# Kernel optimization log

Measured on AMD Instinct MI355X. Metric: run time of the kernel, lower is better.

## Reference

```python
import jax, jax.numpy as jnp
import numpy as np

B, T, IN_CH = 64, 128, 32
H, C = 1, 4
STRIDE = (H, C)
OUT_CH = 4
CHANNELS = (IN_CH - C) // STRIDE[1] + 1  # 8
SIG_DEPTH = 4
D = CHANNELS + 1  # +1 time channel -> 9
LAYERS = (512, 256)
OUT_DIM = 10
SIG_CHANNELS = sum(D ** k for k in range(1, SIG_DEPTH + 1))  # 7380


def _signature(path, depth):
    """Truncated path signature (basepoint=True). path: [N, L, d] -> [N, sum_k d^k].
    Chen's identity scan: S <- S (tensor-mult) exp(dx), levels kept flattened."""
    N, L, d = path.shape
    # basepoint=True: path is prepended with zeros, so first increment is path[:, 0]
    inc = jnp.concatenate([path[:, :1], jnp.diff(path, axis=1)], axis=1)  # [N, L, d]
    inc = jnp.transpose(inc, (1, 0, 2))  # [L, N, d] scan axis first

    def chen_step(S, dx):
        # exponential of the increment: E_k = dx^{\otimes k} / k!
        E = [dx]
        for k in range(2, depth + 1):
            E.append((E[-1][:, :, None] * dx[:, None, :]).reshape(N, -1) / k)
        # Chen: S'_k = S_k + E_k + sum_{j=1}^{k-1} S_j (x) E_{k-j}
        newS = []
        for k in range(1, depth + 1):
            acc = S[k - 1] + E[k - 1]
            for j in range(1, k):
                acc = acc + (S[j - 1][:, :, None] * E[k - 1 - j][:, None, :]).reshape(N, -1)
            newS.append(acc)
        return tuple(newS), None

    S0 = tuple(jnp.zeros((N, d ** k), path.dtype) for k in range(1, depth + 1))
    S, _ = jax.lax.scan(chen_step, S0, inc)
    return jnp.concatenate(S, axis=1)  # [N, SIG_CHANNELS]


def _forward(x, conv_w, conv_b, w0, b0, w1, b1, w2, b2):
    y = jax.lax.conv_general_dilated(
        x, conv_w, window_strides=STRIDE, padding='VALID',
        dimension_numbers=('NCHW', 'OIHW', 'NCHW'))
    y = y + conv_b[None, :, None, None]            # [B, OUT_CH, T', CHANNELS]
    Tp = y.shape[2]
    y = y.reshape(-1, Tp, CHANNELS)                # [B*OUT_CH, T', CHANNELS]
    # signatory.Augment(layer_sizes=(), include_time=True): prepend time channel
    time = jnp.broadcast_to(
        jnp.linspace(0.0, 1.0, Tp, dtype=y.dtype)[None, :, None],
        (y.shape[0], Tp, 1))
    y = jnp.concatenate([time, y], axis=2)         # [B*OUT_CH, T', D]
    sig = _signature(y, SIG_DEPTH)                 # [B*OUT_CH, SIG_CHANNELS]
    z = sig.reshape(-1, OUT_CH * SIG_CHANNELS)     # [B, OUT_CH*SIG_CHANNELS]
    z = jax.nn.sigmoid(z @ w0 + b0)                # dropout = identity (eval mode)
    z = jax.nn.sigmoid(z @ w1 + b1)
    return jax.nn.log_softmax(z @ w2 + b2, axis=1)


def setup_inputs() -> dict:
    key = jax.random.key(0)
    ks = jax.random.split(key, 8)
    x = jax.random.normal(ks[0], (B, 1, T, IN_CH), jnp.float32)
    conv_w = jax.random.normal(ks[1], (OUT_CH, 1, H, C), jnp.float32) * (2.0 / (H * C)) ** 0.5
    conv_b = jnp.zeros((OUT_CH,), jnp.float32)
    dims = [OUT_CH * SIG_CHANNELS] + list(LAYERS) + [OUT_DIM]
    out = {"x": x, "conv_w": conv_w, "conv_b": conv_b}
    for i in range(3):
        out[f"w{i}"] = jax.random.normal(ks[2 + i], (dims[i], dims[i + 1]), jnp.float32) * (2.0 / dims[i]) ** 0.5
        out[f"b{i}"] = jnp.zeros((dims[i + 1],), jnp.float32)
    return out


def reference(x, conv_w, conv_b, w0, b0, w1, b1, w2, b2):
    return _forward(x, conv_w, conv_b, w0, b0, w1, b1, w2, b2)
```

## Files before the change

### kernel.cpp

```cpp
#include <hip/hip_runtime.h>
#include <hip/hip_bf16.h>
#include <math.h>

#define TT 128
#define IN_CH 32
#define NPATH 256
#define SIGCH 7380
#define K1 29520
#define N1 512
#define N2 256

typedef __attribute__((ext_vector_type(8))) short bf16x8;
typedef __attribute__((ext_vector_type(4))) float f32x4;

static __device__ __forceinline__ unsigned pack2bf(float a, float b) {
    union { __hip_bfloat162 h2; unsigned u; } cv;
    cv.h2.x = __float2bfloat16(a);
    cv.h2.y = __float2bfloat16(b);
    return cv.u;
}

__global__ __launch_bounds__(512, 1) void sig_kernel(const float* __restrict__ x,
        const float* __restrict__ cw, const float* __restrict__ cb,
        float* __restrict__ sig ) {
    __shared__ float incT[9][132];
    __shared__ __align__(16) float sb1[12];
    __shared__ __align__(16) float sb2[9][12];
    __shared__ __align__(16) float sb3[81][12];
    __shared__ __align__(16) float sb4[729][12];
    const int p = blockIdx.x;
    const int b = p >> 2, oc = p & 3;
    const int tid = threadIdx.x;

    const float4 wv = *(const float4*)(cw + oc * 4);
    const float bias = cb[oc];
    const float* xb = x + (long)b * TT * IN_CH;

    for (int it = tid; it < TT * 8; it += 512) {
        const int t = it >> 3, ch = it & 7;
        const float4 xa = *(const float4*)(xb + t * IN_CH + ch * 4);
        float v = xa.x * wv.x + xa.y * wv.y + xa.z * wv.z + xa.w * wv.w + bias;
        if (t > 0) {
            const float4 xm = *(const float4*)(xb + (t - 1) * IN_CH + ch * 4);
            v -= xm.x * wv.x + xm.y * wv.y + xm.z * wv.z + xm.w * wv.w + bias;
        }
        incT[1 + ch][t] = v;
    }
    if (tid < TT) incT[0][tid] = tid ? (1.f / 127.f) : 0.f;
    __syncthreads();

    const int g = tid >> 8;
    const int gtid = tid & 255;
    const bool act = gtid < 243;
    const int base3 = 3 * gtid;
    const int i1 = base3 / 81;
    const int i2 = (base3 / 9) % 9;
    const int i30 = base3 % 9;

    float S4[3][9] = {};
    float s3[3] = {0.f, 0.f, 0.f};
    float s2 = 0.f, s1 = 0.f;

#define LD(R, T4) (*(const float4*)&incT[(R)][(T4)])
#define STEP4(CMP) do { \
    const float E1 = e1v.CMP, E2 = e2v.CMP; \
    const float F0 = f0v.CMP, F1 = f1v.CMP, F2 = f2v.CMP; \
    const float t12 = E1 * E2; \
    const float s1d2 = s1 * E2; \
    const float Ak = t12 * (1.f / 24.f) + s1d2 * (1.f / 6.f) + s2 * 0.5f; \
    const float Bk = t12 * (1.f / 6.f) + s1d2 * 0.5f + s2; \
    const float K0 = F0 * Ak + s3[0]; \
    const float K1v = F1 * Ak + s3[1]; \
    const float K2v = F2 * Ak + s3[2]; \
    _Pragma("unroll") \
    for (int c = 0; c < 9; ++c) { \
        const float Ac = A4[c].CMP; \
        S4[0][c] += K0 * Ac; S4[1][c] += K1v * Ac; S4[2][c] += K2v * Ac; \
    } \
    s3[0] += Bk * F0; s3[1] += Bk * F1; s3[2] += Bk * F2; \
    s2 += E2 * (0.5f * E1 + s1); \
    s1 += E1; \
} while (0)

    if (act) {
        const int t0g = g * 64;
        for (int gg = 0; gg < 16; ++gg) {
            const int t4 = t0g + gg * 4;
            float4 A4[9];
#pragma unroll
            for (int c = 0; c < 9; ++c) A4[c] = LD(c, t4);
            const float4 e1v = LD(i1, t4), e2v = LD(i2, t4);
            const float4 f0v = LD(i30, t4), f1v = LD(i30 + 1, t4), f2v = LD(i30 + 2, t4);
            STEP4(x); STEP4(y); STEP4(z); STEP4(w);
        }
    }
#undef STEP4
#undef LD

    if (act && g == 1) {
        if (i2 == 0 && i30 == 0) sb1[i1] = s1;
        if (i30 == 0) sb2[i1][i2] = s2;
#pragma unroll
        for (int q = 0; q < 3; ++q) sb3[i1 * 9 + i2][i30 + q] = s3[q];
#pragma unroll
        for (int q = 0; q < 3; ++q)
#pragma unroll
            for (int c = 0; c < 9; ++c) sb4[base3 + q][c] = S4[q][c];
    }
    __syncthreads();

    if (act && g == 0) {
        float S1B[9];
#pragma unroll
        for (int c = 0; c < 9; ++c) S1B[c] = sb1[c];
#pragma unroll
        for (int q = 0; q < 3; ++q) {
            const float* r2 = sb2[i30 + q];
            const float* r3 = sb3[i2 * 9 + i30 + q];
            const float* r4 = sb4[base3 + q];
#pragma unroll
            for (int c = 0; c < 9; ++c)
                S4[q][c] += s3[q] * S1B[c] + s2 * r2[c] + s1 * r3[c] + r4[c];
        }
#pragma unroll
        for (int q = 0; q < 3; ++q)
            s3[q] += s2 * S1B[i30 + q] + s1 * sb2[i2][i30 + q] + sb3[i1 * 9 + i2][i30 + q];
        s2 += s1 * S1B[i2] + sb2[i1][i2];
        s1 += S1B[i1];

        float* sp = sig + (long)p * SIGCH;
        if (i2 == 0 && i30 == 0) sp[i1] = s1;
        if (i30 == 0) sp[9 + base3 / 9] = s2;
        sp[90 + base3 + 0] = s3[0];
        sp[90 + base3 + 1] = s3[1];
        sp[90 + base3 + 2] = s3[2];
#pragma unroll
        for (int q = 0; q < 3; q++)
#pragma unroll
            for (int l = 0; l < 9; l++)
                sp[819 + (base3 + q) * 9 + l] = S4[q][l];
    }
}

__global__ __launch_bounds__(256) void gemm1_kernel(const float* __restrict__ zsig,
        const float* __restrict__ w0, float* __restrict__ part, int nsub) {
    __shared__ unsigned short za[64][136];
    __shared__ unsigned short wb[64][136];
    const int nq = blockIdx.x;
    const int kc = blockIdx.y;
    const int n0 = nq * 64;
    const int tid = threadIdx.x;
    const int lane = tid & 63;
    const int wvid = __builtin_amdgcn_readfirstlane(tid >> 6);
    const int r0 = wvid * 16;
    const int rA = lane & 15, gr = lane >> 4;

    {
        const int row = tid >> 2, off = 120 + 2 * (tid & 3);
        *(unsigned*)&za[row][off] = 0u;
        *(unsigned*)&wb[row][off] = 0u;
    }

    f32x4 acc[4];
#pragma unroll
    for (int t = 0; t < 4; ++t) acc[t] = (f32x4){0.f, 0.f, 0.f, 0.f};

    for (int s = 0; s < nsub; ++s) {
        const int kb = (blockIdx.y * nsub + s) * 120;
        if (s) __syncthreads();
#pragma unroll
        for (int j = 0; j < 16; ++j) {
            const int i = tid + j * 256;
            const int row = i >> 6, kp = i & 63;
            if (kp < 60) {
                const float2 v = *(const float2*)(zsig + (long)row * K1 + kb + 2 * kp);
                *(unsigned*)&za[row][2 * kp] = pack2bf(v.x, v.y);
            }
        }
#pragma unroll
        for (int j = 0; j < 16; ++j) {
            const int i = tid + j * 256;
            const int c = i & 63, kq = i >> 6;
            if (kq < 60) {
                const float a = w0[(long)(kb + 2 * kq) * N1 + n0 + c];
                const float bvl = w0[(long)(kb + 2 * kq + 1) * N1 + n0 + c];
                *(unsigned*)&wb[c][2 * kq] = pack2bf(a, bvl);
            }
        }
        __syncthreads();
#pragma unroll
        for (int ks = 0; ks < 4; ++ks) {
            const bf16x8 af = *(const bf16x8*)&za[r0 + rA][ks * 32 + gr * 8];
#pragma unroll
            for (int t = 0; t < 4; ++t) {
                const bf16x8 bf = *(const bf16x8*)&wb[16 * t + rA][ks * 32 + gr * 8];
                acc[t] = __builtin_amdgcn_mfma_f32_16x16x32_bf16(af, bf, acc[t], 0, 0, 0);
            }
        }
    }

    float* pp = part + ((long)blockIdx.y * 64 + r0 + 4 * gr) * N1 + n0 + rA;
#pragma unroll
    for (int t = 0; t < 4; ++t)
#pragma unroll
        for (int j = 0; j < 4; ++j)
            pp[(long)j * N1 + 16 * t] = acc[t][j];
}

__global__ __launch_bounds__(256) void red1_kernel(const float* __restrict__ part,
        const float* __restrict__ b0v, float* __restrict__ z1, int ksplit) {
    __shared__ float4 red[256];
    const int tid = threadIdx.x;
    const int cellL = tid & 15, slice = tid >> 4;
    const int cell = blockIdx.x * 16 + cellL;
    const int per = (ksplit + 15) >> 4;
    const int ks = slice * per, ke = min(ksplit, ks + per);
    float4 a = make_float4(0.f, 0.f, 0.f, 0.f);
    for (int kc = ks; kc < ke; kc++) {
        const float4 pv = *(const float4*)(part + ((long)kc * 8192 + cell) * 4);
        a.x += pv.x; a.y += pv.y; a.z += pv.z; a.w += pv.w;
    }
    red[tid] = a;
    __syncthreads();
    if (tid < 128) { float4 o = red[tid + 128]; red[tid].x += o.x; red[tid].y += o.y; red[tid].z += o.z; red[tid].w += o.w; }
    __syncthreads();
    if (tid < 64) { float4 o = red[tid + 64]; red[tid].x += o.x; red[tid].y += o.y; red[tid].z += o.z; red[tid].w += o.w; }
    __syncthreads();
    if (tid < 32) { float4 o = red[tid + 32]; red[tid].x += o.x; red[tid].y += o.y; red[tid].z += o.z; red[tid].w += o.w; }
    __syncthreads();
    if (tid < 16) {
        float4 sum = red[tid];
        float4 o = red[tid + 16];
        sum.x += o.x; sum.y += o.y; sum.z += o.z; sum.w += o.w;
        const float4 bv = *(const float4*)(b0v + (cell & 127) * 4);
        float4 r;
        r.x = 1.f / (1.f + expf(-(sum.x + bv.x)));
        r.y = 1.f / (1.f + expf(-(sum.y + bv.y)));
        r.z = 1.f / (1.f + expf(-(sum.z + bv.z)));
        r.w = 1.f / (1.f + expf(-(sum.w + bv.w)));
        *(float4*)(z1 + cell * 4) = r;
    }
}

__global__ __launch_bounds__(256) void gemm2_kernel(const float* __restrict__ z1,
        const float* __restrict__ w1, const float* __restrict__ b1v,
        float* __restrict__ z2) {
    __shared__ float red[256];
    const int m = blockIdx.x >> 2, nq = blockIdx.x & 3;
    const int tid = threadIdx.x;
    const int c = tid & 63, s = tid >> 6;
    const int n = nq * 64 + c;
    const float* zr = z1 + m * N1 + s * 128;
    const float* wr = w1 + (long)(s * 128) * N2 + n;
    float acc = 0.f;
#pragma unroll 16
    for (int k = 0; k < 128; k++) acc += zr[k] * wr[(long)k * N2];
    red[tid] = acc;
    __syncthreads();
    if (tid < 128) red[tid] += red[tid + 128];
    __syncthreads();
    if (tid < 64) {
        float sum = red[tid] + red[tid + 64] + b1v[n];
        z2[m * N2 + n] = 1.f / (1.f + expf(-sum));
    }
}

__global__ __launch_bounds__(64) void head_kernel(const float* __restrict__ z2,
        const float* __restrict__ w2, const float* __restrict__ b2v,
        float* __restrict__ out) {
    const int m = blockIdx.x;
    const int tid = threadIdx.x;
    __shared__ float logits[10];
    if (tid < 10) {
        float s = b2v[tid];
        const float* zr = z2 + m * N2;
#pragma unroll 8
        for (int k = 0; k < N2; k++) s += zr[k] * w2[k * 10 + tid];
        logits[tid] = s;
    }
    __syncthreads();
    if (tid == 0) {
        float mx = logits[0];
        for (int j = 1; j < 10; j++) mx = fmaxf(mx, logits[j]);
        float sum = 0.f;
        for (int j = 0; j < 10; j++) sum += expf(logits[j] - mx);
        const float lse = mx + logf(sum);
        for (int j = 0; j < 10; j++) out[m * 10 + j] = logits[j] - lse;
    }
}

extern "C" void kernel_launch(void* const* d_in, const int* in_sizes, int n_in,
                              void* d_out, int out_size, void* d_ws, size_t ws_size,
                              hipStream_t stream) {
    const float* x  = (const float*)d_in[0];
    const float* cw = (const float*)d_in[1];
    const float* cb = (const float*)d_in[2];
    const float* w0 = (const float*)d_in[3];
    const float* b0 = (const float*)d_in[4];
    const float* w1 = (const float*)d_in[5];
    const float* b1 = (const float*)d_in[6];
    const float* w2 = (const float*)d_in[7];
    const float* b2 = (const float*)d_in[8];

    const size_t fixed = (size_t)NPATH * SIGCH + 64 * N1 + 64 * N2;
    int ksplit = 41, nsub = 6;
    if (ws_size >= (fixed + (size_t)123 * 64 * N1) * 4)      { ksplit = 123; nsub = 2; }
    else if (ws_size >= (fixed + (size_t)82 * 64 * N1) * 4)  { ksplit = 82;  nsub = 3; }

    float* ws   = (float*)d_ws;
    float* sigb = ws;
    float* part = sigb + (long)NPATH * SIGCH;
    float* z1   = part + (long)ksplit * 64 * N1;
    float* z2   = z1 + 64 * N1;
    float* out  = (float*)d_out;

    sig_kernel<<<NPATH, 512, 0, stream>>>(x, cw, cb, sigb);
    gemm1_kernel<<<dim3(8, ksplit), 256, 0, stream>>>(sigb, w0, part, nsub);
    red1_kernel<<<512, 256, 0, stream>>>(part, b0, z1, ksplit);
    gemm2_kernel<<<256, 256, 0, stream>>>(z1, w1, b1, z2);
    head_kernel<<<64, 64, 0, stream>>>(z2, w2, b2, out);
}
```

Measured before the change: 68.83 us.

## Split signature scan into four time chunks merged via Chen identity kernel

The single per-path signature kernel, which split time into two halves across 512 threads, is replaced by a scan kernel over four 32-step time chunks (1024 blocks of 256 threads) that writes partial signatures to workspace. A new merge kernel then combines the four partials sequentially with Chen's identity. This aims to raise parallelism and occupancy across the GPU's compute units, at the cost of an extra launch, extra global traffic for partial signatures, and three merge rounds instead of one. Workspace use grows, which may push the gemm split choice toward a smaller ksplit.

```diff
diff --git a/kernel.cpp b/kernel.cpp
--- a/kernel.cpp
+++ b/kernel.cpp
@@ -6,6 +6,7 @@
 #define IN_CH 32
 #define NPATH 256
 #define SIGCH 7380
+#define SIGP 7392
 #define K1 29520
 #define N1 512
 #define N2 256
@@ -20,37 +21,35 @@
     return cv.u;
 }
 
-__global__ __launch_bounds__(512, 1) void sig_kernel(const float* __restrict__ x,
+__global__ __launch_bounds__(256) void sigscan_kernel(const float* __restrict__ x,
         const float* __restrict__ cw, const float* __restrict__ cb,
-        float* __restrict__ sig ) {
-    __shared__ float incT[9][132];
-    __shared__ __align__(16) float sb1[12];
-    __shared__ __align__(16) float sb2[9][12];
-    __shared__ __align__(16) float sb3[81][12];
-    __shared__ __align__(16) float sb4[729][12];
+        float* __restrict__ psig ) {
+    __shared__ float incT[9][36];
     const int p = blockIdx.x;
+    const int q4 = blockIdx.y;
     const int b = p >> 2, oc = p & 3;
     const int tid = threadIdx.x;
 
     const float4 wv = *(const float4*)(cw + oc * 4);
     const float bias = cb[oc];
     const float* xb = x + (long)b * TT * IN_CH;
-
-    for (int it = tid; it < TT * 8; it += 512) {
-        const int t = it >> 3, ch = it & 7;
+    const int t0 = q4 * 32;
+
+    {
+        const int tl = tid >> 3, ch = tid & 7;
+        const int t = t0 + tl;
         const float4 xa = *(const float4*)(xb + t * IN_CH + ch * 4);
         float v = xa.x * wv.x + xa.y * wv.y + xa.z * wv.z + xa.w * wv.w + bias;
         if (t > 0) {
             const float4 xm = *(const float4*)(xb + (t - 1) * IN_CH + ch * 4);
             v -= xm.x * wv.x + xm.y * wv.y + xm.z * wv.z + xm.w * wv.w + bias;
         }
-        incT[1 + ch][t] = v;
-    }
-    if (tid < TT) incT[0][tid] = tid ? (1.f / 127.f) : 0.f;
-    __syncthreads();
-
-    const int g = tid >> 8;
-    const int gtid = tid & 255;
+        incT[1 + ch][tl] = v;
+        if (tid < 32) incT[0][tid] = (t0 + tid) ? (1.f / 127.f) : 0.f;
+    }
+    __syncthreads();
+
+    const int gtid = tid;
     const bool act = gtid < 243;
     const int base3 = 3 * gtid;
     const int i1 = base3 / 81;
@@ -83,9 +82,8 @@
 } while (0)
 
     if (act) {
-        const int t0g = g * 64;
-        for (int gg = 0; gg < 16; ++gg) {
-            const int t4 = t0g + gg * 4;
+        for (int gg = 0; gg < 8; ++gg) {
+            const int t4 = gg * 4;
             float4 A4[9];
 #pragma unroll
             for (int c = 0; c < 9; ++c) A4[c] = LD(c, t4);
@@ -93,41 +91,78 @@
             const float4 f0v = LD(i30, t4), f1v = LD(i30 + 1, t4), f2v = LD(i30 + 2, t4);
             STEP4(x); STEP4(y); STEP4(z); STEP4(w);
         }
+        float* d = psig + (long)(p * 4 + q4) * SIGP;
+        if (i2 == 0 && i30 == 0) d[i1] = s1;
+        if (i30 == 0) d[9 + i1 * 9 + i2] = s2;
+        d[90 + base3 + 0] = s3[0];
+        d[90 + base3 + 1] = s3[1];
+        d[90 + base3 + 2] = s3[2];
+#pragma unroll
+        for (int qq = 0; qq < 3; ++qq)
+#pragma unroll
+            for (int c = 0; c < 9; ++c)
+                d[819 + (base3 + qq) * 9 + c] = S4[qq][c];
     }
 #undef STEP4
 #undef LD
-
-    if (act && g == 1) {
-        if (i2 == 0 && i30 == 0) sb1[i1] = s1;
-        if (i30 == 0) sb2[i1][i2] = s2;
-#pragma unroll
-        for (int q = 0; q < 3; ++q) sb3[i1 * 9 + i2][i30 + q] = s3[q];
-#pragma unroll
-        for (int q = 0; q < 3; ++q)
-#pragma unroll
-            for (int c = 0; c < 9; ++c) sb4[base3 + q][c] = S4[q][c];
-    }
-    __syncthreads();
-
-    if (act && g == 0) {
-        float S1B[9];
-#pragma unroll
-        for (int c = 0; c < 9; ++c) S1B[c] = sb1[c];
-#pragma unroll
-        for (int q = 0; q < 3; ++q) {
-            const float* r2 = sb2[i30 + q];
-            const float* r3 = sb3[i2 * 9 + i30 + q];
-            const float* r4 = sb4[base3 + q];
+}
+
+__global__ __launch_bounds__(256) void sigmerge_kernel(const float* __restrict__ psig,
+        float* __restrict__ sig ) {
+    __shared__ float sbuf[SIGP];
+    const int p = blockIdx.x;
+    const int tid = threadIdx.x;
+    const bool act = tid < 243;
+    const int base3 = 3 * tid;
+    const int i1 = base3 / 81;
+    const int i2 = (base3 / 9) % 9;
+    const int i30 = base3 % 9;
+
+    float S4[3][9];
+    float s3[3], s2 = 0.f, s1 = 0.f;
+
+    const float* pA = psig + (long)(p * 4) * SIGP;
+    if (act) {
+        s1 = pA[i1];
+        s2 = pA[9 + i1 * 9 + i2];
+#pragma unroll
+        for (int qq = 0; qq < 3; ++qq) s3[qq] = pA[90 + base3 + qq];
+#pragma unroll
+        for (int qq = 0; qq < 3; ++qq)
 #pragma unroll
             for (int c = 0; c < 9; ++c)
-                S4[q][c] += s3[q] * S1B[c] + s2 * r2[c] + s1 * r3[c] + r4[c];
-        }
-#pragma unroll
-        for (int q = 0; q < 3; ++q)
-            s3[q] += s2 * S1B[i30 + q] + s1 * sb2[i2][i30 + q] + sb3[i1 * 9 + i2][i30 + q];
-        s2 += s1 * S1B[i2] + sb2[i1][i2];
-        s1 += S1B[i1];
-
+                S4[qq][c] = pA[819 + (base3 + qq) * 9 + c];
+    }
+
+    for (int r = 1; r < 4; ++r) {
+        __syncthreads();
+        const float* pB = psig + (long)(p * 4 + r) * SIGP;
+        for (int i = tid; i < SIGP / 4; i += 256)
+            *(float4*)&sbuf[i * 4] = *(const float4*)(pB + i * 4);
+        __syncthreads();
+        if (act) {
+            float S1B[9];
+#pragma unroll
+            for (int c = 0; c < 9; ++c) S1B[c] = sbuf[c];
+#pragma unroll
+            for (int qq = 0; qq < 3; ++qq) {
+                const float* r2 = &sbuf[9 + (i30 + qq) * 9];
+                const float* r3 = &sbuf[90 + (i2 * 9 + i30 + qq) * 9];
+                const float* r4 = &sbuf[819 + (base3 + qq) * 9];
+#pragma unroll
+                for (int c = 0; c < 9; ++c)
+                    S4[qq][c] += s3[qq] * S1B[c] + s2 * r2[c] + s1 * r3[c] + r4[c];
+            }
+#pragma unroll
+            for (int qq = 0; qq < 3; ++qq)
+                s3[qq] += s2 * S1B[i30 + qq] + s1 * sbuf[9 + i2 * 9 + i30 + qq]
+                        + sbuf[90 + (i1 * 9 + i2) * 9 + i30 + qq];
+            s2 += s1 * S1B[i2] + sbuf[9 + i1 * 9 + i2];
+            s1 += S1B[i1];
+        }
+    }
+
+    if (act) {
         float* sp = sig + (long)p * SIGCH;
         if (i2 == 0 && i30 == 0) sp[i1] = s1;
         if (i30 == 0) sp[9 + base3 / 9] = s2;
@@ -135,10 +170,10 @@
         sp[90 + base3 + 1] = s3[1];
         sp[90 + base3 + 2] = s3[2];
 #pragma unroll
-        for (int q = 0; q < 3; q++)
+        for (int qq = 0; qq < 3; qq++)
 #pragma unroll
             for (int l = 0; l < 9; l++)
-                sp[819 + (base3 + q) * 9 + l] = S4[q][l];
+                sp[819 + (base3 + qq) * 9 + l] = S4[qq][l];
     }
 }
 
@@ -147,7 +182,6 @@
     __shared__ unsigned short za[64][136];
     __shared__ unsigned short wb[64][136];
     const int nq = blockIdx.x;
-    const int kc = blockIdx.y;
     const int n0 = nq * 64;
     const int tid = threadIdx.x;
     const int lane = tid & 63;
@@ -302,19 +336,22 @@
     const float* w2 = (const float*)d_in[7];
     const float* b2 = (const float*)d_in[8];
 
-    const size_t fixed = (size_t)NPATH * SIGCH + 64 * N1 + 64 * N2;
+    const size_t fixed = (size_t)NPATH * SIGCH + (size_t)NPATH * 4 * SIGP
+                       + 64 * N1 + 64 * N2;
     int ksplit = 41, nsub = 6;
     if (ws_size >= (fixed + (size_t)123 * 64 * N1) * 4)      { ksplit = 123; nsub = 2; }
     else if (ws_size >= (fixed + (size_t)82 * 64 * N1) * 4)  { ksplit = 82;  nsub = 3; }
 
     float* ws   = (float*)d_ws;
     float* sigb = ws;
-    float* part = sigb + (long)NPATH * SIGCH;
+    float* psig = sigb + (long)NPATH * SIGCH;
+    float* part = psig + (long)NPATH * 4 * SIGP;
     float* z1   = part + (long)ksplit * 64 * N1;
     float* z2   = z1 + 64 * N1;
     float* out  = (float*)d_out;
 
-    sig_kernel<<<NPATH, 512, 0, stream>>>(x, cw, cb, sigb);
+    sigscan_kernel<<<dim3(NPATH, 4), 256, 0, stream>>>(x, cw, cb, psig);
+    sigmerge_kernel<<<NPATH, 256, 0, stream>>>(psig, sigb);
     gemm1_kernel<<<dim3(8, ksplit), 256, 0, stream>>>(sigb, w0, part, nsub);
     red1_kernel<<<512, 256, 0, stream>>>(part, b0, z1, ksplit);
     gemm2_kernel<<<256, 256, 0, stream>>>(z1, w1, b1, z2);
```

Measured after the change: 83.56 us. 21.4% more time.

## Store signatures as bf16, vectorize gemm1 loads, fuse gemm2 and head

Applied to the files above, without the earlier changes.

The signature kernel now writes its output as bf16 instead of fp32. This halves the intermediate buffer and lets gemm1 copy 16-byte chunks straight into shared memory without a per-element convert. The w0 staging now uses float4 loads across columns instead of scalar loads. gemm2 and the head are merged into one tail kernel per batch row, which saves a launch and the z2 round trip but gives each block a longer serial loop over k. The bf16 rounding now happens earlier, which matches the rounding gemm1 already applied.

```diff
diff --git a/kernel.cpp b/kernel.cpp
--- a/kernel.cpp
+++ b/kernel.cpp
@@ -11,6 +11,7 @@
 #define N2 256
 
 typedef __attribute__((ext_vector_type(8))) short bf16x8;
+typedef __attribute__((ext_vector_type(8))) unsigned short u16x8;
 typedef __attribute__((ext_vector_type(4))) float f32x4;
 
 static __device__ __forceinline__ unsigned pack2bf(float a, float b) {
@@ -22,7 +23,7 @@
 
 __global__ __launch_bounds__(512, 1) void sig_kernel(const float* __restrict__ x,
         const float* __restrict__ cw, const float* __restrict__ cb,
-        float* __restrict__ sig ) {
+        __hip_bfloat16* __restrict__ sigbf ) {
     __shared__ float incT[9][132];
     __shared__ __align__(16) float sb1[12];
     __shared__ __align__(16) float sb2[9][12];
@@ -128,26 +129,25 @@
         s2 += s1 * S1B[i2] + sb2[i1][i2];
         s1 += S1B[i1];
 
-        float* sp = sig + (long)p * SIGCH;
-        if (i2 == 0 && i30 == 0) sp[i1] = s1;
-        if (i30 == 0) sp[9 + base3 / 9] = s2;
-        sp[90 + base3 + 0] = s3[0];
-        sp[90 + base3 + 1] = s3[1];
-        sp[90 + base3 + 2] = s3[2];
+        __hip_bfloat16* sp = sigbf + (long)p * SIGCH;
+        if (i2 == 0 && i30 == 0) sp[i1] = __float2bfloat16(s1);
+        if (i30 == 0) sp[9 + base3 / 9] = __float2bfloat16(s2);
+        sp[90 + base3 + 0] = __float2bfloat16(s3[0]);
+        sp[90 + base3 + 1] = __float2bfloat16(s3[1]);
+        sp[90 + base3 + 2] = __float2bfloat16(s3[2]);
 #pragma unroll
         for (int q = 0; q < 3; q++)
 #pragma unroll
             for (int l = 0; l < 9; l++)
-                sp[819 + (base3 + q) * 9 + l] = S4[q][l];
-    }
-}
-
-__global__ __launch_bounds__(256) void gemm1_kernel(const float* __restrict__ zsig,
+                sp[819 + (base3 + q) * 9 + l] = __float2bfloat16(S4[q][l]);
+    }
+}
+
+__global__ __launch_bounds__(256) void gemm1_kernel(const unsigned short* __restrict__ zsig,
         const float* __restrict__ w0, float* __restrict__ part, int nsub) {
     __shared__ unsigned short za[64][136];
     __shared__ unsigned short wb[64][136];
     const int nq = blockIdx.x;
-    const int kc = blockIdx.y;
     const int n0 = nq * 64;
     const int tid = threadIdx.x;
     const int lane = tid & 63;
@@ -169,22 +169,25 @@
         const int kb = (blockIdx.y * nsub + s) * 120;
         if (s) __syncthreads();
 #pragma unroll
-        for (int j = 0; j < 16; ++j) {
+        for (int j = 0; j < 4; ++j) {
             const int i = tid + j * 256;
-            const int row = i >> 6, kp = i & 63;
-            if (kp < 60) {
-                const float2 v = *(const float2*)(zsig + (long)row * K1 + kb + 2 * kp);
-                *(unsigned*)&za[row][2 * kp] = pack2bf(v.x, v.y);
+            if (i < 960) {
+                const int row = i / 15, seg = i % 15;
+                *(u16x8*)&za[row][seg * 8] =
+                    *(const u16x8*)(zsig + (long)row * K1 + kb + seg * 8);
             }
         }
 #pragma unroll
-        for (int j = 0; j < 16; ++j) {
+        for (int j = 0; j < 4; ++j) {
             const int i = tid + j * 256;
-            const int c = i & 63, kq = i >> 6;
-            if (kq < 60) {
-                const float a = w0[(long)(kb + 2 * kq) * N1 + n0 + c];
-                const float bvl = w0[(long)(kb + 2 * kq + 1) * N1 + n0 + c];
-                *(unsigned*)&wb[c][2 * kq] = pack2bf(a, bvl);
+            if (i < 960) {
+                const int kp = i >> 4, cq = (i & 15) * 4;
+                const float4 ra = *(const float4*)(w0 + (long)(kb + 2 * kp) * N1 + n0 + cq);
+                const float4 rb = *(const float4*)(w0 + (long)(kb + 2 * kp + 1) * N1 + n0 + cq);
+                *(unsigned*)&wb[cq + 0][2 * kp] = pack2bf(ra.x, rb.x);
+                *(unsigned*)&wb[cq + 1][2 * kp] = pack2bf(ra.y, rb.y);
+                *(unsigned*)&wb[cq + 2][2 * kp] = pack2bf(ra.z, rb.z);
+                *(unsigned*)&wb[cq + 3][2 * kp] = pack2bf(ra.w, rb.w);
             }
         }
         __syncthreads();
@@ -242,41 +245,37 @@
     }
 }
 
-__global__ __launch_bounds__(256) void gemm2_kernel(const float* __restrict__ z1,
+__global__ __launch_bounds__(256) void tail_kernel(const float* __restrict__ z1,
         const float* __restrict__ w1, const float* __restrict__ b1v,
-        float* __restrict__ z2) {
-    __shared__ float red[256];
-    const int m = blockIdx.x >> 2, nq = blockIdx.x & 3;
-    const int tid = threadIdx.x;
-    const int c = tid & 63, s = tid >> 6;
-    const int n = nq * 64 + c;
-    const float* zr = z1 + m * N1 + s * 128;
-    const float* wr = w1 + (long)(s * 128) * N2 + n;
-    float acc = 0.f;
-#pragma unroll 16
-    for (int k = 0; k < 128; k++) acc += zr[k] * wr[(long)k * N2];
-    red[tid] = acc;
-    __syncthreads();
-    if (tid < 128) red[tid] += red[tid + 128];
-    __syncthreads();
-    if (tid < 64) {
-        float sum = red[tid] + red[tid + 64] + b1v[n];
-        z2[m * N2 + n] = 1.f / (1.f + expf(-sum));
-    }
-}
-
-__global__ __launch_bounds__(64) void head_kernel(const float* __restrict__ z2,
         const float* __restrict__ w2, const float* __restrict__ b2v,
         float* __restrict__ out) {
+    __shared__ float z2row[N2];
+    __shared__ float red[160];
+    __shared__ float logits[10];
     const int m = blockIdx.x;
     const int tid = threadIdx.x;
-    __shared__ float logits[10];
+    const float* zr = z1 + m * N1;
+    float acc = b1v[tid];
+#pragma unroll 8
+    for (int k = 0; k < N1; k++) acc += zr[k] * w1[(long)k * N2 + tid];
+    z2row[tid] = 1.f / (1.f + expf(-acc));
+    __syncthreads();
+    if (tid < 160) {
+        const int j = tid >> 4, s = tid & 15;
+        float p = 0.f;
+#pragma unroll
+        for (int kk = 0; kk < 16; kk++) {
+            const int k = s * 16 + kk;
+            p += z2row[k] * w2[k * 10 + j];
+        }
+        red[tid] = p;
+    }
+    __syncthreads();
     if (tid < 10) {
-        float s = b2v[tid];
-        const float* zr = z2 + m * N2;
-#pragma unroll 8
-        for (int k = 0; k < N2; k++) s += zr[k] * w2[k * 10 + tid];
-        logits[tid] = s;
+        float lg = b2v[tid];
+#pragma unroll
+        for (int s = 0; s < 16; s++) lg += red[tid * 16 + s];
+        logits[tid] = lg;
     }
     __syncthreads();
     if (tid == 0) {
@@ -302,21 +301,20 @@
     const float* w2 = (const float*)d_in[7];
     const float* b2 = (const float*)d_in[8];
 
-    const size_t fixed = (size_t)NPATH * SIGCH + 64 * N1 + 64 * N2;
+    const size_t sig_floats = (size_t)NPATH * SIGCH / 2;
+    const size_t fixed = sig_floats + 64 * N1 + 64 * N2;
     int ksplit = 41, nsub = 6;
     if (ws_size >= (fixed + (size_t)123 * 64 * N1) * 4)      { ksplit = 123; nsub = 2; }
     else if (ws_size >= (fixed + (size_t)82 * 64 * N1) * 4)  { ksplit = 82;  nsub = 3; }
 
     float* ws   = (float*)d_ws;
-    float* sigb = ws;
-    float* part = sigb + (long)NPATH * SIGCH;
+    unsigned short* sigbf = (unsigned short*)ws;
+    float* part = ws + sig_floats;
     float* z1   = part + (long)ksplit * 64 * N1;
-    float* z2   = z1 + 64 * N1;
     float* out  = (float*)d_out;
 
-    sig_kernel<<<NPATH, 512, 0, stream>>>(x, cw, cb, sigb);
-    gemm1_kernel<<<dim3(8, ksplit), 256, 0, stream>>>(sigb, w0, part, nsub);
+    sig_kernel<<<NPATH, 512, 0, stream>>>(x, cw, cb, (__hip_bfloat16*)sigbf);
+    gemm1_kernel<<<dim3(8, ksplit), 256, 0, stream>>>(sigbf, w0, part, nsub);
     red1_kernel<<<512, 256, 0, stream>>>(part, b0, z1, ksplit);
-    gemm2_kernel<<<256, 256, 0, stream>>>(z1, w1, b1, z2);
-    head_kernel<<<64, 64, 0, stream>>>(z2, w2, b2, out);
-}
+    tail_kernel<<<64, 256, 0, stream>>>(z1, w1, b1, w2, b2, out);
+}
```

Result: slower. 72.37 us (+5.1%).

## Emit signature as bf16 via shared staging and vectorize GEMM1 tile loads

Applied to the files above, without the earlier changes.

The signature kernel now writes its final levels back into shared memory and then stores them to global memory as packed bf16 pairs with coalesced writes. This halves the signature buffer size and removes the fp32-to-bf16 conversion from the GEMM1 A-tile load, which becomes 16-byte vector copies. The w0 B-tile load now uses float4 reads and packs four columns per thread instead of scalar loads. The cost is two extra block barriers and index-decoding work in the signature kernel's store loop.

```diff
diff --git a/kernel.cpp b/kernel.cpp
--- a/kernel.cpp
+++ b/kernel.cpp
@@ -11,6 +11,7 @@
 #define N2 256
 
 typedef __attribute__((ext_vector_type(8))) short bf16x8;
+typedef __attribute__((ext_vector_type(8))) unsigned short u16x8;
 typedef __attribute__((ext_vector_type(4))) float f32x4;
 
 static __device__ __forceinline__ unsigned pack2bf(float a, float b) {
@@ -22,7 +23,7 @@
 
 __global__ __launch_bounds__(512, 1) void sig_kernel(const float* __restrict__ x,
         const float* __restrict__ cw, const float* __restrict__ cb,
-        float* __restrict__ sig ) {
+        __hip_bfloat16* __restrict__ sigbf ) {
     __shared__ float incT[9][132];
     __shared__ __align__(16) float sb1[12];
     __shared__ __align__(16) float sb2[9][12];
@@ -127,27 +128,45 @@
             s3[q] += s2 * S1B[i30 + q] + s1 * sb2[i2][i30 + q] + sb3[i1 * 9 + i2][i30 + q];
         s2 += s1 * S1B[i2] + sb2[i1][i2];
         s1 += S1B[i1];
-
-        float* sp = sig + (long)p * SIGCH;
-        if (i2 == 0 && i30 == 0) sp[i1] = s1;
-        if (i30 == 0) sp[9 + base3 / 9] = s2;
-        sp[90 + base3 + 0] = s3[0];
-        sp[90 + base3 + 1] = s3[1];
-        sp[90 + base3 + 2] = s3[2];
-#pragma unroll
-        for (int q = 0; q < 3; q++)
-#pragma unroll
-            for (int l = 0; l < 9; l++)
-                sp[819 + (base3 + q) * 9 + l] = S4[q][l];
-    }
-}
-
-__global__ __launch_bounds__(256) void gemm1_kernel(const float* __restrict__ zsig,
+    }
+    __syncthreads();
+
+    if (act && g == 0) {
+        if (i2 == 0 && i30 == 0) sb1[i1] = s1;
+        if (i30 == 0) sb2[i1][i2] = s2;
+#pragma unroll
+        for (int q = 0; q < 3; ++q) sb3[i1 * 9 + i2][i30 + q] = s3[q];
+#pragma unroll
+        for (int q = 0; q < 3; ++q)
+#pragma unroll
+            for (int c = 0; c < 9; ++c) sb4[base3 + q][c] = S4[q][c];
+    }
+    __syncthreads();
+
+    {
+        unsigned* sp = (unsigned*)(sigbf + (long)p * SIGCH);
+        for (int j = tid; j < SIGCH / 2; j += 512) {
+            const int idx = 2 * j;
+            float v0, v1;
+#define RD(IDX, V) do { \
+            const int ix_ = (IDX); \
+            if (ix_ < 9) V = sb1[ix_]; \
+            else if (ix_ < 90) { const int jj = ix_ - 9;  V = sb2[jj / 9][jj % 9]; } \
+            else if (ix_ < 819) { const int jj = ix_ - 90; V = sb3[jj / 9][jj % 9]; } \
+            else { const int jj = ix_ - 819; V = sb4[jj / 9][jj % 9]; } } while (0)
+            RD(idx, v0);
+            RD(idx + 1, v1);
+#undef RD
+            sp[j] = pack2bf(v0, v1);
+        }
+    }
+}
+
+__global__ __launch_bounds__(256) void gemm1_kernel(const unsigned short* __restrict__ zsig,
         const float* __restrict__ w0, float* __restrict__ part, int nsub) {
     __shared__ unsigned short za[64][136];
     __shared__ unsigned short wb[64][136];
     const int nq = blockIdx.x;
-    const int kc = blockIdx.y;
     const int n0 = nq * 64;
     const int tid = threadIdx.x;
     const int lane = tid & 63;
@@ -169,22 +188,25 @@
         const int kb = (blockIdx.y * nsub + s) * 120;
         if (s) __syncthreads();
 #pragma unroll
-        for (int j = 0; j < 16; ++j) {
+        for (int j = 0; j < 4; ++j) {
             const int i = tid + j * 256;
-            const int row = i >> 6, kp = i & 63;
-            if (kp < 60) {
-                const float2 v = *(const float2*)(zsig + (long)row * K1 + kb + 2 * kp);
-                *(unsigned*)&za[row][2 * kp] = pack2bf(v.x, v.y);
+            if (i < 960) {
+                const int row = i / 15, seg = i % 15;
+                *(u16x8*)&za[row][seg * 8] =
+                    *(const u16x8*)(zsig + (long)row * K1 + kb + seg * 8);
             }
         }
 #pragma unroll
-        for (int j = 0; j < 16; ++j) {
+        for (int j = 0; j < 4; ++j) {
             const int i = tid + j * 256;
-            const int c = i & 63, kq = i >> 6;
-            if (kq < 60) {
-                const float a = w0[(long)(kb + 2 * kq) * N1 + n0 + c];
-                const float bvl = w0[(long)(kb + 2 * kq + 1) * N1 + n0 + c];
-                *(unsigned*)&wb[c][2 * kq] = pack2bf(a, bvl);
+            if (i < 960) {
+                const int kp = i >> 4, cq = (i & 15) * 4;
+                const float4 ra = *(const float4*)(w0 + (long)(kb + 2 * kp) * N1 + n0 + cq);
+                const float4 rb = *(const float4*)(w0 + (long)(kb + 2 * kp + 1) * N1 + n0 + cq);
+                *(unsigned*)&wb[cq + 0][2 * kp] = pack2bf(ra.x, rb.x);
+                *(unsigned*)&wb[cq + 1][2 * kp] = pack2bf(ra.y, rb.y);
+                *(unsigned*)&wb[cq + 2][2 * kp] = pack2bf(ra.z, rb.z);
+                *(unsigned*)&wb[cq + 3][2 * kp] = pack2bf(ra.w, rb.w);
             }
         }
         __syncthreads();
@@ -302,20 +324,21 @@
     const float* w2 = (const float*)d_in[7];
     const float* b2 = (const float*)d_in[8];
 
-    const size_t fixed = (size_t)NPATH * SIGCH + 64 * N1 + 64 * N2;
+    const size_t sig_floats = (size_t)NPATH * SIGCH / 2;
+    const size_t fixed = sig_floats + 64 * N1 + 64 * N2;
     int ksplit = 41, nsub = 6;
     if (ws_size >= (fixed + (size_t)123 * 64 * N1) * 4)      { ksplit = 123; nsub = 2; }
     else if (ws_size >= (fixed + (size_t)82 * 64 * N1) * 4)  { ksplit = 82;  nsub = 3; }
 
     float* ws   = (float*)d_ws;
-    float* sigb = ws;
-    float* part = sigb + (long)NPATH * SIGCH;
+    unsigned short* sigbf = (unsigned short*)ws;
+    float* part = ws + sig_floats;
     float* z1   = part + (long)ksplit * 64 * N1;
     float* z2   = z1 + 64 * N1;
     float* out  = (float*)d_out;
 
-    sig_kernel<<<NPATH, 512, 0, stream>>>(x, cw, cb, sigb);
-    gemm1_kernel<<<dim3(8, ksplit), 256, 0, stream>>>(sigb, w0, part, nsub);
+    sig_kernel<<<NPATH, 512, 0, stream>>>(x, cw, cb, (__hip_bfloat16*)sigbf);
+    gemm1_kernel<<<dim3(8, ksplit), 256, 0, stream>>>(sigbf, w0, part, nsub);
     red1_kernel<<<512, 256, 0, stream>>>(part, b0, z1, ksplit);
     gemm2_kernel<<<256, 256, 0, stream>>>(z1, w1, b1, z2);
     head_kernel<<<64, 64, 0, stream>>>(z2, w2, b2, out);
```

After: 63.40 us. 1.09x faster.
